# Performance work log

Measured on AMD Instinct MI355X. Metric: run time of the kernel, lower is better.

## Reference

```python
import jax, jax.numpy as jnp
import numpy as np

B, T, NCH, NBIN, NBAND = 2, 400, 8, 512, 40
NPV = NCH * NCH


def setup_inputs() -> dict:
    key = jax.random.key(0)
    ks = jax.random.split(key, 7)
    bins_real = jax.random.normal(ks[0], (B, T, NCH, NBIN), jnp.float32)
    bins_imag = jax.random.normal(ks[1], (B, T, NCH, NBIN), jnp.float32)
    band_matrix_real = jax.random.normal(ks[2], (NBIN, NBAND), jnp.float32) * 0.05
    band_matrix_imag = jax.random.normal(ks[3], (NBIN, NBAND), jnp.float32) * 0.05
    cov_to_pv_real = jax.random.normal(ks[4], (NPV, NCH * NCH), jnp.float32) * 0.1
    cov_to_pv_imag = jax.random.normal(ks[5], (NPV, NCH * NCH), jnp.float32) * 0.1
    tau = jax.random.uniform(ks[6], (NBAND,), jnp.float32, 0.8, 0.99)
    return {
        'bins_real': bins_real, 'bins_imag': bins_imag,
        'band_matrix_real': band_matrix_real, 'band_matrix_imag': band_matrix_imag,
        'cov_to_pv_real': cov_to_pv_real, 'cov_to_pv_imag': cov_to_pv_imag,
        'tau': tau,
    }


def _power_vector(bins_real, bins_imag, band_matrix_real, band_matrix_imag,
                  cov_to_pv_real, cov_to_pv_imag, tau):
    x = jax.lax.complex(bins_real, bins_imag)            # (B,T,C,F)
    nch = x.shape[-2]
    EPS = 1e-20
    # per-bin covariance outer product, flattened cov dim: (B,T,F,C*C)
    cov = jnp.einsum('btif,btjf->btfij', x, jnp.conj(x))
    b, t, f = cov.shape[:3]
    cov = cov.reshape(b, t, f, nch * nch)
    diag = jnp.arange(nch) * (nch + 1)                   # diagonal indices in cov dim
    trace = jnp.clip(jnp.sum(cov.real[..., diag], axis=-1, keepdims=True), EPS, None)
    cov = cov / trace                                    # per-bin trace normalisation
    # phase adjustment along the bin axis (n=1 -> lag of 2 bins)
    c = jnp.swapaxes(cov, -1, -2)                        # (B,T,C2,F)
    prod = jnp.conj(c[..., :-2]) * c[..., 2:]
    ang = jnp.arctan2(prod.imag, prod.real)
    ang = jnp.concatenate([ang[..., :1], ang, ang[..., -1:]], axis=-1)  # edge pad
    adj = jnp.abs(c) * jax.lax.complex(jnp.cos(ang), jnp.sin(ang))
    adj = adj.at[..., diag, :].set(c[..., diag, :])      # keep original diagonals
    # band projection: contract bins against (F,K) band matrix
    bm = jax.lax.complex(band_matrix_real, band_matrix_imag)
    band_cov = jnp.einsum('btcf,fk->btkc', adj, bm)      # (B,T,K,C2)
    dsum = jnp.clip(band_cov.real[..., diag].sum(-1, keepdims=True), EPS, None)
    band_cov = band_cov / dsum
    # first-order IIR smoothing over frames, per-band pole tau
    a = tau[:, None].astype(band_cov.real.dtype)         # (K,1)
    def step(carry, xt):
        y = a * carry + (1.0 - a) * xt
        return y, y
    y0 = jnp.zeros_like(band_cov[:, 0])                  # (B,K,C2)
    _, ys = jax.lax.scan(step, y0, jnp.moveaxis(band_cov, 1, 0))
    band_cov = jnp.moveaxis(ys, 0, 1)                    # (B,T,K,C2)
    # cov -> power vector projection, real part
    c2p = jax.lax.complex(cov_to_pv_real, cov_to_pv_imag)  # (P,C2)
    pv = jnp.einsum('pc,btkc->btkp', c2p, band_cov).real   # (B,T,K,P)
    return pv


def reference(bins_real, bins_imag, band_matrix_real, band_matrix_imag,
              cov_to_pv_real, cov_to_pv_imag, tau):
    return _power_vector(bins_real, bins_imag, band_matrix_real, band_matrix_imag,
                         cov_to_pv_real, cov_to_pv_imag, tau)
```

## Files before the change

kernel.cpp:

```cpp
#include <hip/hip_runtime.h>

#define B_    2
#define T_    400
#define NCH_  8
#define NBIN_ 512
#define NBAND_ 40
#define NPV_  64

using short8  = __attribute__((ext_vector_type(8))) short;
using float4v = __attribute__((ext_vector_type(4))) float;

static __device__ inline unsigned pkbf(float x, float y) {
  union { float f; unsigned u; } a, b;
  a.f = x; b.f = y;
  unsigned ra = a.u + 0x7fffu + ((a.u >> 16) & 1u);
  unsigned rb = b.u + 0x7fffu + ((b.u >> 16) & 1u);
  return (ra >> 16) | (rb & 0xffff0000u);
}

__global__ __launch_bounds__(256) void pv_prep(
    const float* __restrict__ bmr, const float* __restrict__ bmi,
    const float* __restrict__ c2pr, const float* __restrict__ c2pi,
    float* __restrict__ ws)
{
  const int tid = threadIdx.x;
  const int blk = blockIdx.x;
  if (blk == 0) {
    __shared__ float sds[256];
    int k = tid & 63, part = tid >> 6;
    float s = 0.f;
    if (k < NBAND_) {
      const float* col = bmr + k;
      #pragma unroll 16
      for (int f = part * 128; f < part * 128 + 128; f++) s += col[f * 40];
    }
    sds[tid] = s;
    __syncthreads();
    if (tid < NBAND_) {
      float t = sds[tid] + sds[tid + 64] + sds[tid + 128] + sds[tid + 192];
      ws[tid] = 1.0f / fmaxf(t, 1e-20f);
    }
  } else if (blk <= 48) {
    int F = (blk - 1) * 256 + tid;
    int l = F & 63;
    int rest = F >> 6;
    int s5 = rest & 31;
    int gn = rest >> 5;
    int n = gn % 3, g = gn / 3;
    int k = n * 16 + (l & 15);
    unsigned dw[4];
    #pragma unroll
    for (int t2 = 0; t2 < 4; t2++) {
      float v0 = 0.f, v1 = 0.f;
      if (k < NBAND_) {
        int kd = s5 * 32 + (l >> 4) * 8 + 2 * t2;
        int f = kd >> 1;
        if (g == 0) { v0 = bmr[f * 40 + k]; v1 = -bmi[f * 40 + k]; }
        else        { v0 = bmi[f * 40 + k]; v1 =  bmr[f * 40 + k]; }
      }
      dw[t2] = pkbf(v0, v1);
    }
    ((uint4*)((char*)ws + 1024))[F] = make_uint4(dw[0], dw[1], dw[2], dw[3]);
  } else {
    int F2 = (blk - 49) * 256 + tid;
    int lane = F2 & 63, E = F2 >> 6;
    int nt = E >> 2, ks = E & 3;
    int n = lane & 15, quad = lane >> 4;
    int p = nt * 16 + n;
    unsigned dw[4];
    #pragma unroll
    for (int t2 = 0; t2 < 4; t2++) {
      int c = ks * 16 + quad * 4 + t2;
      dw[t2] = pkbf(c2pr[p * 64 + c], -c2pi[p * 64 + c]);
    }
    ((uint4*)((char*)ws + 197632))[E * 64 + lane] = make_uint4(dw[0], dw[1], dw[2], dw[3]);
  }
}

__global__ __launch_bounds__(256, 4) void pv_main(
    const float* __restrict__ br, const float* __restrict__ bi,
    const float* __restrict__ ws, float* __restrict__ out)
{
  __shared__ __align__(16) float smem[8224];
  float2* vsh = (float2*)smem;

  const int bt  = blockIdx.x;
  const int tid = threadIdx.x;
  const float* pr  = br + (size_t)bt * (NCH_ * NBIN_);
  const float* pim = bi + (size_t)bt * (NCH_ * NBIN_);

  #pragma unroll
  for (int fs = 0; fs < 2; fs++) {
    const int f = tid + fs * 256;
    const int fm = (f == 0) ? 0 : ((f == 511) ? 509 : f - 1);
    const int fp = (f == 0) ? 2 : ((f == 511) ? 511 : f + 1);
    float tr = 0.f;
    float t1[8], t2[8];
    #pragma unroll
    for (int c = 0; c < 8; c++) {
      const float* cr = pr + c * 512;
      const float* ci = pim + c * 512;
      float xr = cr[f],   xi = ci[f];
      float xrm = cr[fm], xim = ci[fm];
      float xrp = cr[fp], xip = ci[fp];
      tr = fmaf(xr, xr, tr); tr = fmaf(xi, xi, tr);
      float Gr = fmaf(xrm, xrp,  xim * xip);
      float Gi = fmaf(xrm, xip, -(xim * xrp));
      float am = fmaxf(fmaxf(fabsf(Gr), fabsf(Gi)), 1e-30f);
      float rc = __builtin_amdgcn_rcpf(am);
      float q1 = Gr * rc, q2 = Gi * rc;
      float n2 = fmaf(q1, q1, q2 * q2);
      float rn = __builtin_amdgcn_rsqf(n2);
      bool ok = n2 > 0.f;
      float ur = ok ? q1 * rn : 1.f;
      float ui = ok ? q2 * rn : 0.f;
      float mg = __builtin_amdgcn_sqrtf(fmaf(xr, xr, xi * xi));
      t1[c] = mg * ur; t2[c] = mg * ui;
    }
    float scv = __builtin_amdgcn_rsqf(fmaxf(tr, 1e-20f));
    #pragma unroll
    for (int c = 0; c < 8; c++)
      vsh[c * 514 + f] = make_float2(t1[c] * scv, t2[c] * scv);
  }
  __syncthreads();

  const int w    = tid >> 6;
  const int lane = tid & 63;
  const int m16  = lane & 15;
  const int quad = lane >> 4;
  const int p    = w * 16 + m16;
  const int ich  = p >> 3, jch = p & 7;
  const float4* Av = (const float4*)(vsh + ich * 514 + quad * 4);
  const float4* Bv = (const float4*)(vsh + jch * 514 + quad * 4);
  const float4* BF = ((const float4*)((const char*)ws + 1024)) + lane;

  float4v acc[6];
  #pragma unroll
  for (int g = 0; g < 6; g++) acc[g] = (float4v){0.f, 0.f, 0.f, 0.f};

  float4 curB[6], nxtB[6];
  #pragma unroll
  for (int g = 0; g < 6; g++) curB[g] = BF[(g * 32) * 64];

  #pragma unroll 2
  for (int s = 0; s < 32; s++) {
    if (s < 31) {
      #pragma unroll
      for (int g = 0; g < 6; g++) nxtB[g] = BF[(g * 32 + s + 1) * 64];
    }
    float4 a01 = Av[s * 8], a23 = Av[s * 8 + 1];
    float4 b01 = Bv[s * 8], b23 = Bv[s * 8 + 1];
    float ar0 = fmaf(a01.x, b01.x,  a01.y * b01.y);
    float ai0 = fmaf(a01.y, b01.x, -(a01.x * b01.y));
    float ar1 = fmaf(a01.z, b01.z,  a01.w * b01.w);
    float ai1 = fmaf(a01.w, b01.z, -(a01.z * b01.w));
    float ar2 = fmaf(a23.x, b23.x,  a23.y * b23.y);
    float ai2 = fmaf(a23.y, b23.x, -(a23.x * b23.y));
    float ar3 = fmaf(a23.z, b23.z,  a23.w * b23.w);
    float ai3 = fmaf(a23.w, b23.z, -(a23.z * b23.w));
    uint4 au = make_uint4(pkbf(ar0, ai0), pkbf(ar1, ai1),
                          pkbf(ar2, ai2), pkbf(ar3, ai3));
    short8 afrag = __builtin_bit_cast(short8, au);
    #pragma unroll
    for (int g = 0; g < 6; g++) {
      short8 bfrag = __builtin_bit_cast(short8, curB[g]);
      acc[g] = __builtin_amdgcn_mfma_f32_16x16x32_bf16(afrag, bfrag, acc[g], 0, 0, 0);
    }
    #pragma unroll
    for (int g = 0; g < 6; g++) curB[g] = nxtB[g];
  }

  const uint4* EF = ((const uint4*)((const char*)ws + 197632)) + (w * 4) * 64 + lane;
  uint4 eb[4];
  #pragma unroll
  for (int ks = 0; ks < 4; ks++) eb[ks] = EF[ks * 64];

  __syncthreads();
  float2* bcsh = (float2*)smem;
  float*  dssh = smem + 6336;
  #pragma unroll
  for (int n = 0; n < 3; n++) {
    int k = n * 16 + m16;
    #pragma unroll
    for (int r = 0; r < 4; r++) {
      int c = w * 16 + quad * 4 + r;
      bcsh[k * 66 + c] = make_float2(acc[n][r], acc[3 + n][r]);
    }
  }
  if (tid < 48) dssh[tid] = (tid < NBAND_) ? ws[tid] : 0.f;
  __syncthreads();

  float4v eacc[3];
  #pragma unroll
  for (int mt = 0; mt < 3; mt++) eacc[mt] = (float4v){0.f, 0.f, 0.f, 0.f};
  #pragma unroll
  for (int ks = 0; ks < 4; ks++) {
    short8 bfrag = __builtin_bit_cast(short8, eb[ks]);
    #pragma unroll
    for (int mt = 0; mt < 3; mt++) {
      const float4* Ae = (const float4*)(bcsh + (mt * 16 + m16) * 66 + ks * 16 + quad * 4);
      float4 w0 = Ae[0], w1 = Ae[1];
      uint4 au2 = make_uint4(pkbf(w0.x, w0.y), pkbf(w0.z, w0.w),
                             pkbf(w1.x, w1.y), pkbf(w1.z, w1.w));
      short8 af2 = __builtin_bit_cast(short8, au2);
      eacc[mt] = __builtin_amdgcn_mfma_f32_16x16x32_bf16(af2, bfrag, eacc[mt], 0, 0, 0);
    }
  }
  float* op = out + (size_t)bt * (NBAND_ * NPV_);
  #pragma unroll
  for (int mt = 0; mt < 3; mt++) {
    const float4* dv4 = (const float4*)(dssh + mt * 16 + quad * 4);
    float4 dv = dv4[0];
    float dva[4] = {dv.x, dv.y, dv.z, dv.w};
    #pragma unroll
    for (int r = 0; r < 4; r++) {
      int k = mt * 16 + quad * 4 + r;
      if (k < NBAND_)
        op[k * 64 + w * 16 + m16] = eacc[mt][r] * dva[r];
    }
  }
}

__global__ __launch_bounds__(256) void pv_iir3(float* __restrict__ z,
                                               const float* __restrict__ tau)
{
  __shared__ float gsh[16][16];
  const int pg = blockIdx.x & 3;
  const int bk = blockIdx.x >> 2;
  const int k = bk % NBAND_;
  const int b = bk / NBAND_;
  const float a  = tau[k];
  const float om = 1.0f - a;
  const int c  = threadIdx.x >> 4;
  const int pl = threadIdx.x & 15;
  const int p  = pg * 16 + pl;
  const size_t stride = (size_t)NBAND_ * 64;
  size_t idx0 = (size_t)b * (T_ * NBAND_ * 64) + (size_t)(c * 25) * stride + k * 64 + p;

  float y[25];
  float accv = 0.f;
  #pragma unroll
  for (int i = 0; i < 25; i++) {
    float v = z[idx0 + (size_t)i * stride];
    accv = fmaf(a, accv, om * v);
    y[i] = accv;
  }
  gsh[c][pl] = accv;
  __syncthreads();
  float a2 = a * a, a8 = a2 * a2 * a2 * a2, a16 = a8 * a8;
  float A = a16 * a8 * a;
  float H = 0.f;
  #pragma unroll
  for (int d = 0; d < 15; d++) {
    if (d < c) H = fmaf(A, H, gsh[d][pl]);
  }
  float wp = a;
  #pragma unroll
  for (int i = 0; i < 25; i++) {
    z[idx0 + (size_t)i * stride] = fmaf(wp, H, y[i]);
    wp *= a;
  }
}

extern "C" void kernel_launch(void* const* d_in, const int* in_sizes, int n_in,
                              void* d_out, int out_size, void* d_ws, size_t ws_size,
                              hipStream_t stream)
{
  const float* br   = (const float*)d_in[0];
  const float* bi   = (const float*)d_in[1];
  const float* bmr  = (const float*)d_in[2];
  const float* bmi  = (const float*)d_in[3];
  const float* c2pr = (const float*)d_in[4];
  const float* c2pi = (const float*)d_in[5];
  const float* tau  = (const float*)d_in[6];
  float* out = (float*)d_out;
  float* ws  = (float*)d_ws;

  hipLaunchKernelGGL(pv_prep, dim3(53), dim3(256), 0, stream,
                     bmr, bmi, c2pr, c2pi, ws);
  hipLaunchKernelGGL(pv_main, dim3(B_ * T_), dim3(256), 0, stream,
                     br, bi, ws, out);
  hipLaunchKernelGGL(pv_iir3, dim3(B_ * NBAND_ * 4), dim3(256), 0, stream,
                     out, tau);
}
```

Measured before the change: 122.9 us.

## Split pv_main K-loop across two wave groups with bf16 shared staging

Doubles the block to 512 threads so each thread computes one bin in the prologue, and splits the 32-step bin contraction into two halves run by separate wave groups. The partial accumulators are reduced through shared memory before the second projection. The per-bin adjusted values and band covariances are stored in shared memory as packed bf16 instead of float2, which shrinks LDS traffic and removes the software prefetch of B fragments. The cost is an extra reduction pass and barrier, plus half the waves sitting idle during the final projection.

```diff
diff --git a/kernel.cpp b/kernel.cpp
--- a/kernel.cpp
+++ b/kernel.cpp
@@ -16,6 +16,11 @@
   unsigned ra = a.u + 0x7fffu + ((a.u >> 16) & 1u);
   unsigned rb = b.u + 0x7fffu + ((b.u >> 16) & 1u);
   return (ra >> 16) | (rb & 0xffff0000u);
+}
+static __device__ inline void upk(unsigned u, float& lo, float& hi) {
+  union { unsigned q; float f; } a, b;
+  a.q = u << 16; b.q = u & 0xffff0000u;
+  lo = a.f; hi = b.f;
 }
 
 __global__ __launch_bounds__(256) void pv_prep(
@@ -77,21 +82,22 @@
   }
 }
 
-__global__ __launch_bounds__(256, 4) void pv_main(
+__global__ __launch_bounds__(512, 6) void pv_main(
     const float* __restrict__ br, const float* __restrict__ bi,
     const float* __restrict__ ws, float* __restrict__ out)
 {
-  __shared__ __align__(16) float smem[8224];
-  float2* vsh = (float2*)smem;
+  __shared__ __align__(16) unsigned smem[10320];
+  unsigned* vsh  = smem;
+  float*    red  = (float*)(smem + 4128);
+  float*    dssh = (float*)(smem + 10272);
 
   const int bt  = blockIdx.x;
   const int tid = threadIdx.x;
   const float* pr  = br + (size_t)bt * (NCH_ * NBIN_);
   const float* pim = bi + (size_t)bt * (NCH_ * NBIN_);
 
-  #pragma unroll
-  for (int fs = 0; fs < 2; fs++) {
-    const int f = tid + fs * 256;
+  {
+    const int f = tid;
     const int fm = (f == 0) ? 0 : ((f == 511) ? 509 : f - 1);
     const int fp = (f == 0) ? 2 : ((f == 511) ? 511 : f + 1);
     float tr = 0.f;
@@ -120,103 +126,113 @@
     float scv = __builtin_amdgcn_rsqf(fmaxf(tr, 1e-20f));
     #pragma unroll
     for (int c = 0; c < 8; c++)
-      vsh[c * 514 + f] = make_float2(t1[c] * scv, t2[c] * scv);
+      vsh[c * 516 + f] = pkbf(t1[c] * scv, t2[c] * scv);
   }
   __syncthreads();
 
-  const int w    = tid >> 6;
+  const int wv   = tid >> 6;
+  const int kh   = wv >> 2;
+  const int mt   = wv & 3;
   const int lane = tid & 63;
   const int m16  = lane & 15;
   const int quad = lane >> 4;
-  const int p    = w * 16 + m16;
+  const int p    = mt * 16 + m16;
   const int ich  = p >> 3, jch = p & 7;
-  const float4* Av = (const float4*)(vsh + ich * 514 + quad * 4);
-  const float4* Bv = (const float4*)(vsh + jch * 514 + quad * 4);
-  const float4* BF = ((const float4*)((const char*)ws + 1024)) + lane;
+  const uint4* Avp = (const uint4*)(vsh + ich * 516) + quad;
+  const uint4* Bvp = (const uint4*)(vsh + jch * 516) + quad;
+  const float4* BFl = ((const float4*)((const char*)ws + 1024)) + lane;
 
   float4v acc[6];
   #pragma unroll
   for (int g = 0; g < 6; g++) acc[g] = (float4v){0.f, 0.f, 0.f, 0.f};
 
-  float4 curB[6], nxtB[6];
-  #pragma unroll
-  for (int g = 0; g < 6; g++) curB[g] = BF[(g * 32) * 64];
-
-  #pragma unroll 2
-  for (int s = 0; s < 32; s++) {
-    if (s < 31) {
+  #pragma unroll 4
+  for (int s = 0; s < 16; s++) {
+    const int sg = kh * 16 + s;
+    uint4 av = Avp[sg * 4];
+    uint4 bv = Bvp[sg * 4];
+    float ar[4], ai[4];
+    {
+      float vr, vi, wr, wi;
+      upk(av.x, vr, vi); upk(bv.x, wr, wi);
+      ar[0] = fmaf(vr, wr,  vi * wi); ai[0] = fmaf(vi, wr, -(vr * wi));
+      upk(av.y, vr, vi); upk(bv.y, wr, wi);
+      ar[1] = fmaf(vr, wr,  vi * wi); ai[1] = fmaf(vi, wr, -(vr * wi));
+      upk(av.z, vr, vi); upk(bv.z, wr, wi);
+      ar[2] = fmaf(vr, wr,  vi * wi); ai[2] = fmaf(vi, wr, -(vr * wi));
+      upk(av.w, vr, vi); upk(bv.w, wr, wi);
+      ar[3] = fmaf(vr, wr,  vi * wi); ai[3] = fmaf(vi, wr, -(vr * wi));
+    }
+    uint4 au = make_uint4(pkbf(ar[0], ai[0]), pkbf(ar[1], ai[1]),
+                          pkbf(ar[2], ai[2]), pkbf(ar[3], ai[3]));
+    short8 afrag = __builtin_bit_cast(short8, au);
+    #pragma unroll
+    for (int g = 0; g < 6; g++) {
+      float4 rawb = BFl[(g * 32 + sg) * 64];
+      short8 bfrag = __builtin_bit_cast(short8, rawb);
+      acc[g] = __builtin_amdgcn_mfma_f32_16x16x32_bf16(afrag, bfrag, acc[g], 0, 0, 0);
+    }
+  }
+
+  if (kh == 1) {
+    const int slot = tid & 255;
+    #pragma unroll
+    for (int g = 0; g < 6; g++)
       #pragma unroll
-      for (int g = 0; g < 6; g++) nxtB[g] = BF[(g * 32 + s + 1) * 64];
-    }
-    float4 a01 = Av[s * 8], a23 = Av[s * 8 + 1];
-    float4 b01 = Bv[s * 8], b23 = Bv[s * 8 + 1];
-    float ar0 = fmaf(a01.x, b01.x,  a01.y * b01.y);
-    float ai0 = fmaf(a01.y, b01.x, -(a01.x * b01.y));
-    float ar1 = fmaf(a01.z, b01.z,  a01.w * b01.w);
-    float ai1 = fmaf(a01.w, b01.z, -(a01.z * b01.w));
-    float ar2 = fmaf(a23.x, b23.x,  a23.y * b23.y);
-    float ai2 = fmaf(a23.y, b23.x, -(a23.x * b23.y));
-    float ar3 = fmaf(a23.z, b23.z,  a23.w * b23.w);
-    float ai3 = fmaf(a23.w, b23.z, -(a23.z * b23.w));
-    uint4 au = make_uint4(pkbf(ar0, ai0), pkbf(ar1, ai1),
-                          pkbf(ar2, ai2), pkbf(ar3, ai3));
-    short8 afrag = __builtin_bit_cast(short8, au);
-    #pragma unroll
-    for (int g = 0; g < 6; g++) {
-      short8 bfrag = __builtin_bit_cast(short8, curB[g]);
-      acc[g] = __builtin_amdgcn_mfma_f32_16x16x32_bf16(afrag, bfrag, acc[g], 0, 0, 0);
-    }
-    #pragma unroll
-    for (int g = 0; g < 6; g++) curB[g] = nxtB[g];
-  }
-
-  const uint4* EF = ((const uint4*)((const char*)ws + 197632)) + (w * 4) * 64 + lane;
-  uint4 eb[4];
-  #pragma unroll
-  for (int ks = 0; ks < 4; ks++) eb[ks] = EF[ks * 64];
-
-  __syncthreads();
-  float2* bcsh = (float2*)smem;
-  float*  dssh = smem + 6336;
-  #pragma unroll
-  for (int n = 0; n < 3; n++) {
-    int k = n * 16 + m16;
-    #pragma unroll
-    for (int r = 0; r < 4; r++) {
-      int c = w * 16 + quad * 4 + r;
-      bcsh[k * 66 + c] = make_float2(acc[n][r], acc[3 + n][r]);
-    }
+      for (int r = 0; r < 4; r++)
+        red[(g * 4 + r) * 256 + slot] = acc[g][r];
   }
   if (tid < 48) dssh[tid] = (tid < NBAND_) ? ws[tid] : 0.f;
   __syncthreads();
 
-  float4v eacc[3];
-  #pragma unroll
-  for (int mt = 0; mt < 3; mt++) eacc[mt] = (float4v){0.f, 0.f, 0.f, 0.f};
-  #pragma unroll
-  for (int ks = 0; ks < 4; ks++) {
-    short8 bfrag = __builtin_bit_cast(short8, eb[ks]);
-    #pragma unroll
-    for (int mt = 0; mt < 3; mt++) {
-      const float4* Ae = (const float4*)(bcsh + (mt * 16 + m16) * 66 + ks * 16 + quad * 4);
-      float4 w0 = Ae[0], w1 = Ae[1];
-      uint4 au2 = make_uint4(pkbf(w0.x, w0.y), pkbf(w0.z, w0.w),
-                             pkbf(w1.x, w1.y), pkbf(w1.z, w1.w));
-      short8 af2 = __builtin_bit_cast(short8, au2);
-      eacc[mt] = __builtin_amdgcn_mfma_f32_16x16x32_bf16(af2, bfrag, eacc[mt], 0, 0, 0);
-    }
-  }
-  float* op = out + (size_t)bt * (NBAND_ * NPV_);
-  #pragma unroll
-  for (int mt = 0; mt < 3; mt++) {
-    const float4* dv4 = (const float4*)(dssh + mt * 16 + quad * 4);
-    float4 dv = dv4[0];
-    float dva[4] = {dv.x, dv.y, dv.z, dv.w};
-    #pragma unroll
-    for (int r = 0; r < 4; r++) {
-      int k = mt * 16 + quad * 4 + r;
-      if (k < NBAND_)
-        op[k * 64 + w * 16 + m16] = eacc[mt][r] * dva[r];
+  uint4 eb[4];
+  if (kh == 0) {
+    const int slot = tid;
+    #pragma unroll
+    for (int g = 0; g < 6; g++)
+      #pragma unroll
+      for (int r = 0; r < 4; r++)
+        acc[g][r] += red[(g * 4 + r) * 256 + slot];
+
+    unsigned* bcsh = smem;
+    #pragma unroll
+    for (int n = 0; n < 3; n++) {
+      uint4 w4 = make_uint4(pkbf(acc[n][0], acc[n + 3][0]),
+                            pkbf(acc[n][1], acc[n + 3][1]),
+                            pkbf(acc[n][2], acc[n + 3][2]),
+                            pkbf(acc[n][3], acc[n + 3][3]));
+      *(uint4*)(bcsh + (n * 16 + m16) * 68 + mt * 16 + quad * 4) = w4;
+    }
+    const uint4* EF = ((const uint4*)((const char*)ws + 197632)) + (mt * 4) * 64 + lane;
+    #pragma unroll
+    for (int ks = 0; ks < 4; ks++) eb[ks] = EF[ks * 64];
+  }
+  __syncthreads();
+
+  if (kh == 0) {
+    const unsigned* bcsh = smem;
+    float4v eacc[3];
+    #pragma unroll
+    for (int kt = 0; kt < 3; kt++) eacc[kt] = (float4v){0.f, 0.f, 0.f, 0.f};
+    #pragma unroll
+    for (int ks = 0; ks < 4; ks++) {
+      short8 bfr = __builtin_bit_cast(short8, eb[ks]);
+      #pragma unroll
+      for (int kt = 0; kt < 3; kt++) {
+        uint4 a4 = *(const uint4*)(bcsh + (kt * 16 + m16) * 68 + ks * 16 + quad * 4);
+        short8 afr = __builtin_bit_cast(short8, a4);
+        eacc[kt] = __builtin_amdgcn_mfma_f32_16x16x32_bf16(afr, bfr, eacc[kt], 0, 0, 0);
+      }
+    }
+    float* op = out + (size_t)bt * (NBAND_ * NPV_);
+    #pragma unroll
+    for (int kt = 0; kt < 3; kt++) {
+      #pragma unroll
+      for (int r = 0; r < 4; r++) {
+        int k = kt * 16 + quad * 4 + r;
+        if (k < NBAND_)
+          op[k * 64 + mt * 16 + m16] = eacc[kt][r] * dssh[k];
+      }
     }
   }
 }
@@ -278,7 +294,7 @@
 
   hipLaunchKernelGGL(pv_prep, dim3(53), dim3(256), 0, stream,
                      bmr, bmi, c2pr, c2pi, ws);
-  hipLaunchKernelGGL(pv_main, dim3(B_ * T_), dim3(256), 0, stream,
+  hipLaunchKernelGGL(pv_main, dim3(B_ * T_), dim3(512), 0, stream,
                      br, bi, ws, out);
   hipLaunchKernelGGL(pv_iir3, dim3(B_ * NBAND_ * 4), dim3(256), 0, stream,
                      out, tau);
```

Measured after the change: 134.4 us. +9.3%, slower.
